# Optimization experiments

Hardware: AMD Instinct MI355X
Metric: run time of the kernel (lower is better)

Reference implementation:

```python
import jax, jax.numpy as jnp
import numpy as np

NUM_HEADS = 16


def setup_inputs() -> dict:
    key = jax.random.key(0)
    ks = jax.random.split(key, 7)
    B, S, H = 4, 2048, 1024
    scale = 1.0 / np.sqrt(H)
    return {
        "hidden_states": jax.random.normal(ks[0], (B, S, H), dtype=jnp.float32),
        "attention_mask": jnp.ones((B, S), dtype=jnp.int32),
        "Wq": jax.random.normal(ks[1], (H, H), dtype=jnp.float32) * scale,
        "bq": jnp.zeros((H,), dtype=jnp.float32),
        "Wk": jax.random.normal(ks[2], (H, H), dtype=jnp.float32) * scale,
        "bk": jnp.zeros((H,), dtype=jnp.float32),
        "Wv": jax.random.normal(ks[3], (H, H), dtype=jnp.float32) * scale,
        "bv": jnp.zeros((H,), dtype=jnp.float32),
    }


def _split_heads(x, n_heads):
    B, S, H = x.shape
    return x.reshape(B, S, n_heads, H // n_heads).transpose(0, 2, 1, 3)  # [B,h,S,d]


def reference(hidden_states, attention_mask, Wq, bq, Wk, bk, Wv, bv):
    B, S, H = hidden_states.shape
    dh = H // NUM_HEADS
    # nn.Linear applies x @ W.T + b
    q = _split_heads(hidden_states @ Wq.T + bq, NUM_HEADS)
    k = _split_heads(hidden_states @ Wk.T + bk, NUM_HEADS)
    v = _split_heads(hidden_states @ Wv.T + bv, NUM_HEADS)
    scores = jnp.einsum("bhqd,bhkd->bhqk", q, k)  # [B,h,S,S]
    # masked_fill with -inf before scaling == masking after scaling
    mask = attention_mask[:, None, None, :] == 0
    scores = jnp.where(mask, -jnp.inf, scores)
    probs = jax.nn.softmax(scores / jnp.sqrt(jnp.float32(dh)), axis=-1)
    out = jnp.einsum("bhqk,bhkd->bhqd", probs, v)  # [B,h,S,d]
    return out.transpose(0, 2, 1, 3).reshape(B, S, H)
```

## Files before the change

### kernel.cpp

```cpp
#include <hip/hip_runtime.h>
#include <hip/hip_bf16.h>
#include <stdint.h>

constexpr int CB  = 4;
constexpr int CS  = 2048;
constexpr int CH  = 1024;
constexpr int CNH = 16;
constexpr int CDH = 64;
constexpr int CM  = CB * CS;

typedef __bf16 bf16x8 __attribute__((ext_vector_type(8)));
typedef float  f32x4  __attribute__((ext_vector_type(4)));

__device__ __forceinline__ unsigned short f2bf(float f) {
    union { float f; unsigned u; } c; c.f = f;
    unsigned u = c.u;
    unsigned r = (u + 0x7fffu + ((u >> 16) & 1u)) >> 16;
    return (unsigned short)r;
}

__device__ __forceinline__ void gl_lds16(const void* g, void* l) {
    __builtin_amdgcn_global_load_lds((const __attribute__((address_space(1))) uint32_t*)g,
                                     (__attribute__((address_space(3))) uint32_t*)l,
                                     16, 0, 0);
}

__device__ __forceinline__ float fexp2(float x) {
#if __has_builtin(__builtin_amdgcn_exp2f)
    return __builtin_amdgcn_exp2f(x);
#else
    return exp2f(x);
#endif
}

__device__ __forceinline__ unsigned cvtpk_bf16(float lo, float hi) {
    unsigned r;
    asm("v_cvt_pk_bf16_f32 %0, %1, %2" : "=v"(r) : "v"(lo), "v"(hi));
    return r;
}

__device__ __forceinline__ void pl32swap(unsigned &a, unsigned &b) {
#if __has_builtin(__builtin_amdgcn_permlane32_swap)
    auto r = __builtin_amdgcn_permlane32_swap(a, b, false, false);
    a = r[0]; b = r[1];
#else
    int lane = threadIdx.x & 63;
    unsigned as = (unsigned)__shfl((int)a, lane ^ 32);
    unsigned bs = (unsigned)__shfl((int)b, lane ^ 32);
    unsigned na = (lane < 32) ? a : bs;
    unsigned nb = (lane < 32) ? as : b;
    a = na; b = nb;
#endif
}

__device__ __forceinline__ void pl16swap(unsigned &a, unsigned &b) {
#if __has_builtin(__builtin_amdgcn_permlane16_swap)
    auto r = __builtin_amdgcn_permlane16_swap(a, b, false, false);
    a = r[0]; b = r[1];
#else
    unsigned as = __builtin_amdgcn_ds_swizzle(a, 0x401F);
    unsigned bs = __builtin_amdgcn_ds_swizzle(b, 0x401F);
    int odd = (threadIdx.x >> 4) & 1;
    unsigned na = odd ? bs : a;
    unsigned nb = odd ? b : as;
    a = na; b = nb;
#endif
}

constexpr float C_SC = 0.125f * 1.44269504f;

__global__ __launch_bounds__(256) void cvt_all(const float* __restrict__ hs,
                                               const float* __restrict__ w0,
                                               const float* __restrict__ w1,
                                               const float* __restrict__ w2,
                                               unsigned short* __restrict__ Xb,
                                               unsigned short* __restrict__ Wb) {
    int z = blockIdx.y;
    const float* src; unsigned short* dst; int n4;
    if (z == 0)      { src = hs; dst = Xb;              n4 = CM * CH / 4; }
    else if (z == 1) { src = w0; dst = Wb;              n4 = CH * CH / 4; }
    else if (z == 2) { src = w1; dst = Wb + CH * CH;    n4 = CH * CH / 4; }
    else             { src = w2; dst = Wb + 2 * CH * CH; n4 = CH * CH / 4; }
    int i = blockIdx.x * blockDim.x + threadIdx.x;
    if (i < n4) {
        float4 v = ((const float4*)src)[i];
        ushort4 o;
        o.x = f2bf(v.x); o.y = f2bf(v.y); o.z = f2bf(v.z); o.w = f2bf(v.w);
        ((ushort4*)dst)[i] = o;
    }
}

__global__ __launch_bounds__(256) void qkv_gemm(
    const unsigned short* __restrict__ Xb,
    const unsigned short* __restrict__ Wb,
    const float* __restrict__ bq, const float* __restrict__ bk, const float* __restrict__ bv,
    unsigned short* __restrict__ Qo,
    unsigned short* __restrict__ Ko,
    unsigned short* __restrict__ Vt)
{
    __shared__ alignas(16) unsigned char smem[34816];
    typedef unsigned short (*tile_t)[128][32];
    tile_t As = (tile_t)smem;
    tile_t Bs = (tile_t)(smem + 16384);
    typedef unsigned short (*ep_t)[136];
    ep_t Ep = (ep_t)smem;

    const int tid  = threadIdx.x;
    const int wave = tid >> 6, lane = tid & 63;
    const int wm = wave >> 1, wn = wave & 1;
    const int col = lane & 15, quad = lane >> 4;
    const int gm = blockIdx.x * 128, gn = blockIdx.y * 128;
    const int z  = blockIdx.z;
    const unsigned short* W = Wb + (size_t)z * CH * CH;

    f32x4 zero = {0.f, 0.f, 0.f, 0.f};
    f32x4 acc[4][4];
    for (int i = 0; i < 4; i++) for (int j = 0; j < 4; j++) acc[i][j] = zero;

    const int arow = lane >> 2;
    const int acol = (lane & 3) * 8;

    auto stage = [&](int buf, int k0) {
        for (int c = 0; c < 2; ++c) {
            int r0 = wave * 32 + c * 16;
            gl_lds16(Xb + (size_t)(gm + r0 + arow) * CH + k0 + acol, &As[buf][r0][0]);
            gl_lds16(W  + (size_t)(gn + r0 + arow) * CH + k0 + acol, &Bs[buf][r0][0]);
        }
    };

    stage(0, 0);
    for (int kk = 0; kk < 32; ++kk) {
        int cur = kk & 1;
        __syncthreads();
        if (kk < 31) stage(cur ^ 1, (kk + 1) * 32);
        bf16x8 af[4], bfm[4];
        for (int i = 0; i < 4; i++)
            af[i] = *(const bf16x8*)&As[cur][wm * 64 + i * 16 + col][quad * 8];
        for (int j = 0; j < 4; j++)
            bfm[j] = *(const bf16x8*)&Bs[cur][wn * 64 + j * 16 + col][quad * 8];
        for (int i = 0; i < 4; i++)
            for (int j = 0; j < 4; j++)
                acc[i][j] = __builtin_amdgcn_mfma_f32_16x16x32_bf16(af[i], bfm[j], acc[i][j], 0, 0, 0);
    }

    __syncthreads();

    const float* bias = (z == 0) ? bq : (z == 1) ? bk : bv;
    const int bb = gm >> 11, ss0 = gm & 2047;
    const int h0 = gn >> 6;

    if (z == 2) {
        for (int j = 0; j < 4; j++) {
            int nl = wn * 64 + j * 16 + col;
            float bias_v = bias[gn + nl];
            for (int i = 0; i < 4; i++) {
                int ml = wm * 64 + i * 16 + quad * 4;
                unsigned d0 = (unsigned)f2bf(acc[i][j][0] + bias_v) |
                              ((unsigned)f2bf(acc[i][j][1] + bias_v) << 16);
                unsigned d1 = (unsigned)f2bf(acc[i][j][2] + bias_v) |
                              ((unsigned)f2bf(acc[i][j][3] + bias_v) << 16);
                *(unsigned*)&Ep[nl][ml]     = d0;
                *(unsigned*)&Ep[nl][ml + 2] = d1;
            }
        }
        __syncthreads();
        for (int p = 0; p < 8; p++) {
            int nl = p * 16 + (tid >> 4);
            int seg = tid & 15;
            uint4 v = *(const uint4*)&Ep[nl][seg * 8];
            int h = h0 + (nl >> 6), d = nl & 63;
            *(uint4*)(Vt + ((size_t)(bb * CNH + h) * CDH + d) * CS + ss0 + seg * 8) = v;
        }
    } else {
        const float mulf = (z == 0) ? C_SC : 1.0f;
        for (int j = 0; j < 4; j++) {
            int nl = wn * 64 + j * 16 + col;
            float bias_v = bias[gn + nl];
            for (int i = 0; i < 4; i++)
                for (int r = 0; r < 4; r++) {
                    int ml = wm * 64 + i * 16 + quad * 4 + r;
                    Ep[ml][nl] = f2bf((acc[i][j][r] + bias_v) * mulf);
                }
        }
        __syncthreads();
        unsigned short* dst01 = (z == 0) ? Qo : Ko;
        for (int p = 0; p < 8; p++) {
            int ml = p * 16 + (tid >> 4);
            int half2 = (tid >> 3) & 1, seg = tid & 7;
            uint4 v = *(const uint4*)&Ep[ml][half2 * 64 + seg * 8];
            int h = h0 + half2;
            *(uint4*)(dst01 + ((size_t)(bb * CNH + h) * CS + ss0 + ml) * CDH + seg * 8) = v;
        }
    }
}

__global__ __launch_bounds__(256, 2) void flash_attn(
    const unsigned short* __restrict__ Q,
    const unsigned short* __restrict__ K,
    const unsigned short* __restrict__ Vt,
    const int* __restrict__ mask,
    float* __restrict__ out)
{
    __shared__ alignas(16) unsigned short Ks[3][64][64];
    __shared__ alignas(16) unsigned short Vs[3][64][64];
    __shared__ unsigned int Mbits[64];

    const int tid  = threadIdx.x;
    const int wave = tid >> 6, lane = tid & 63;
    const int col = lane & 15, quad = lane >> 4;

    const int wg   = blockIdx.y * gridDim.x + blockIdx.x;
    const int nid  = (wg & 7) * 64 + (wg >> 3);
    const int bh   = nid >> 3;
    const int qblk = nid & 7;
    const int bI = bh >> 4, hI = bh & 15;
    const int q0 = qblk * 256 + wave * 64;

    const unsigned short* Qp = Q  + (size_t)bh * CS * CDH;
    const unsigned short* Kp = K  + (size_t)bh * CS * CDH;
    const unsigned short* Vp = Vt + (size_t)bh * CDH * CS;

    {
        const int* mg = mask + bI * CS;
        for (int j = 0; j < 8; j++) {
            int idx = wave * 512 + j * 64 + lane;
            unsigned long long bal = __ballot(mg[idx] != 0);
            if (lane == 0) {
                Mbits[wave * 16 + j * 2]     = (unsigned int)bal;
                Mbits[wave * 16 + j * 2 + 1] = (unsigned int)(bal >> 32);
            }
        }
    }

    bf16x8 aq[4][2];
    for (int i = 0; i < 4; i++)
        for (int ks = 0; ks < 2; ks++)
            aq[i][ks] = *(const bf16x8*)(Qp + (size_t)(q0 + i * 16 + col) * CDH + ks * 32 + quad * 8);

    bf16x8 onesb;
    {
        union { unsigned short u; __bf16 b; } ob; ob.u = 0x3F80;
        for (int j = 0; j < 8; j++) onesb[j] = ob.b;
    }

    f32x4 zero = {0.f, 0.f, 0.f, 0.f};
    f32x4 o[4][4], lfr[4];
    for (int i = 0; i < 4; i++) {
        lfr[i] = zero;
        for (int id = 0; id < 4; id++) o[i][id] = zero;
    }

    const int srow = lane >> 3;
    const int schk = (lane & 7) ^ srow;

    auto stageKV = [&](int buf, int t) {
        const unsigned short* kg = Kp + (size_t)t * 64 * CDH;
        for (int c = 0; c < 2; c++) {
            int r0 = wave * 16 + c * 8;
            gl_lds16(kg + (size_t)(r0 + srow) * CDH + schk * 8, &Ks[buf][r0][0]);
            gl_lds16(Vp + (size_t)(r0 + srow) * CS + t * 64 + schk * 8, &Vs[buf][r0][0]);
        }
    };

    stageKV(0, 0);
    stageKV(1, 1);
    asm volatile("s_waitcnt lgkmcnt(0)" ::: "memory");

    int cur = 0, sp = 2;
    for (int kt = 0; kt < 32; ++kt) {
        if (kt < 31) asm volatile("s_waitcnt vmcnt(4)" ::: "memory");
        else         asm volatile("s_waitcnt vmcnt(0)" ::: "memory");
        asm volatile("s_barrier" ::: "memory");
        if (kt < 30) stageKV(sp, kt + 2);

        f32x4 sfr[4][4];
        for (int i = 0; i < 4; i++) for (int ik = 0; ik < 4; ik++) sfr[i][ik] = zero;
        for (int ks = 0; ks < 2; ks++) {
            bf16x8 bkf[4];
            for (int ik = 0; ik < 4; ik++)
                bkf[ik] = *(const bf16x8*)&Ks[cur][ik * 16 + col][((ks * 4 + quad) ^ (col & 7)) * 8];
            __builtin_amdgcn_s_setprio(1);
            for (int i = 0; i < 4; i++)
                for (int ik = 0; ik < 4; ik++)
                    sfr[i][ik] = __builtin_amdgcn_mfma_f32_16x16x32_bf16(bkf[ik], aq[i][ks], sfr[i][ik], 0, 0, 0);
            __builtin_amdgcn_s_setprio(0);
        }

        unsigned int w0 = Mbits[kt * 2], w1 = Mbits[kt * 2 + 1];
        if ((w0 & w1) != 0xFFFFFFFFu) {
            for (int ik = 0; ik < 4; ik++)
                for (int r = 0; r < 4; r++) {
                    int kv = ik * 16 + quad * 4 + r;
                    unsigned bit = (kv < 32) ? (w0 >> kv) : (w1 >> (kv - 32));
                    float madd = (bit & 1u) ? 0.f : -1.0e30f;
                    for (int i = 0; i < 4; i++) sfr[i][ik][r] += madd;
                }
        }

        bf16x8 bvf[2][4];
        for (int ks = 0; ks < 2; ks++)
            for (int id = 0; id < 4; id++)
                bvf[ks][id] = *(const bf16x8*)&Vs[cur][id * 16 + col][((ks * 4 + quad) ^ (col & 7)) * 8];

        for (int i = 0; i < 4; i++) {
            unsigned c[4][2];
            for (int ik = 0; ik < 4; ik++)
                for (int h = 0; h < 2; h++)
                    c[ik][h] = cvtpk_bf16(fexp2(sfr[i][ik][2 * h]), fexp2(sfr[i][ik][2 * h + 1]));

            unsigned a0 = c[0][0], b0 = c[1][0]; pl32swap(a0, b0); pl16swap(a0, b0);
            unsigned a1 = c[0][1], b1 = c[1][1]; pl32swap(a1, b1); pl16swap(a1, b1);
            unsigned a2 = c[2][0], b2 = c[3][0]; pl32swap(a2, b2); pl16swap(a2, b2);
            unsigned a3 = c[2][1], b3 = c[3][1]; pl32swap(a3, b3); pl16swap(a3, b3);

            uint4 lo4; lo4.x = a0; lo4.y = a1; lo4.z = b0; lo4.w = b1;
            uint4 hi4; hi4.x = a2; hi4.y = a3; hi4.z = b2; hi4.w = b3;
            bf16x8 ap0, ap1;
            __builtin_memcpy(&ap0, &lo4, 16);
            __builtin_memcpy(&ap1, &hi4, 16);

            __builtin_amdgcn_s_setprio(1);
            for (int id = 0; id < 4; id++)
                o[i][id] = __builtin_amdgcn_mfma_f32_16x16x32_bf16(ap0, bvf[0][id], o[i][id], 0, 0, 0);
            lfr[i] = __builtin_amdgcn_mfma_f32_16x16x32_bf16(ap0, onesb, lfr[i], 0, 0, 0);
            for (int id = 0; id < 4; id++)
                o[i][id] = __builtin_amdgcn_mfma_f32_16x16x32_bf16(ap1, bvf[1][id], o[i][id], 0, 0, 0);
            lfr[i] = __builtin_amdgcn_mfma_f32_16x16x32_bf16(ap1, onesb, lfr[i], 0, 0, 0);
            __builtin_amdgcn_s_setprio(0);
        }

        cur = (cur + 1 == 3) ? 0 : cur + 1;
        sp  = (sp  + 1 == 3) ? 0 : sp  + 1;
    }

    for (int i = 0; i < 4; i++)
        for (int r = 0; r < 4; r++) {
            int sI = q0 + i * 16 + quad * 4 + r;
            float inv = 1.0f / lfr[i][r];
            for (int id = 0; id < 4; id++)
                out[((size_t)(bI * CS + sI)) * CH + hI * CDH + id * 16 + col] = o[i][id][r] * inv;
        }
}

extern "C" void kernel_launch(void* const* d_in, const int* in_sizes, int n_in,
                              void* d_out, int out_size, void* d_ws, size_t ws_size,
                              hipStream_t stream) {
    const float* hs  = (const float*)d_in[0];
    const int*  mask = (const int*)d_in[1];
    const float* Wq  = (const float*)d_in[2];
    const float* bq  = (const float*)d_in[3];
    const float* Wk  = (const float*)d_in[4];
    const float* bk  = (const float*)d_in[5];
    const float* Wv  = (const float*)d_in[6];
    const float* bv  = (const float*)d_in[7];
    float* out = (float*)d_out;

    char* ws = (char*)d_ws;
    unsigned short* Xb = (unsigned short*)(ws);
    unsigned short* Wb = (unsigned short*)(ws + 16777216);
    unsigned short* Qb = (unsigned short*)(ws + 23068672);
    unsigned short* Kb = (unsigned short*)(ws + 39845888);
    unsigned short* Vt = (unsigned short*)(ws + 56623104);

    cvt_all<<<dim3(8192, 4), 256, 0, stream>>>(hs, Wq, Wk, Wv, Xb, Wb);

    qkv_gemm<<<dim3(CM / 128, CH / 128, 3), 256, 0, stream>>>(Xb, Wb, bq, bk, bv, Qb, Kb, Vt);

    flash_attn<<<dim3(8, 64), 256, 0, stream>>>(Qb, Kb, Vt, mask, out);
}
```

Measured before the change: 250.8 us.

## Load K/V fragments directly from global into registers, dropping LDS staging

The flash-attention kernel no longer stages K and V tiles through a triple-buffered LDS ring with global_load_lds and barriers. Each wave now loads its MFMA K and V fragments straight from global memory (L2) into registers, software-pipelined so that the next tile's QK^T is issued at the end of the current iteration. This removes LDS traffic and per-tile block barriers. In exchange, the four waves in a block each fetch the same K/V data separately, which raises L2/global load traffic and register pressure.

```diff
diff --git a/kernel.cpp b/kernel.cpp
--- a/kernel.cpp
+++ b/kernel.cpp
@@ -201,8 +201,6 @@
     const int* __restrict__ mask,
     float* __restrict__ out)
 {
-    __shared__ alignas(16) unsigned short Ks[3][64][64];
-    __shared__ alignas(16) unsigned short Vs[3][64][64];
     __shared__ unsigned int Mbits[64];
 
     const int tid  = threadIdx.x;
@@ -216,9 +214,9 @@
     const int bI = bh >> 4, hI = bh & 15;
     const int q0 = qblk * 256 + wave * 64;
 
-    const unsigned short* Qp = Q  + (size_t)bh * CS * CDH;
-    const unsigned short* Kp = K  + (size_t)bh * CS * CDH;
-    const unsigned short* Vp = Vt + (size_t)bh * CDH * CS;
+    const unsigned short* Qp = Q + (size_t)bh * CS * CDH;
+    const char* Kp8 = (const char*)(K  + (size_t)bh * CS * CDH);
+    const char* Vp8 = (const char*)(Vt + (size_t)bh * CDH * CS);
 
     {
         const int* mg = mask + bI * CS;
@@ -231,80 +229,104 @@
             }
         }
     }
+    __syncthreads();
 
     bf16x8 aq[4][2];
+    #pragma unroll
     for (int i = 0; i < 4; i++)
+        #pragma unroll
         for (int ks = 0; ks < 2; ks++)
             aq[i][ks] = *(const bf16x8*)(Qp + (size_t)(q0 + i * 16 + col) * CDH + ks * 32 + quad * 8);
 
     bf16x8 onesb;
     {
         union { unsigned short u; __bf16 b; } ob; ob.u = 0x3F80;
+        #pragma unroll
         for (int j = 0; j < 8; j++) onesb[j] = ob.b;
     }
 
     f32x4 zero = {0.f, 0.f, 0.f, 0.f};
     f32x4 o[4][4], lfr[4];
+    #pragma unroll
     for (int i = 0; i < 4; i++) {
         lfr[i] = zero;
+        #pragma unroll
         for (int id = 0; id < 4; id++) o[i][id] = zero;
     }
 
-    const int srow = lane >> 3;
-    const int schk = (lane & 7) ^ srow;
-
-    auto stageKV = [&](int buf, int t) {
-        const unsigned short* kg = Kp + (size_t)t * 64 * CDH;
-        for (int c = 0; c < 2; c++) {
-            int r0 = wave * 16 + c * 8;
-            gl_lds16(kg + (size_t)(r0 + srow) * CDH + schk * 8, &Ks[buf][r0][0]);
-            gl_lds16(Vp + (size_t)(r0 + srow) * CS + t * 64 + schk * 8, &Vs[buf][r0][0]);
-        }
+    unsigned voKa = (unsigned)(col * 128 + quad * 16);
+    unsigned voKb = voKa + 4096u;
+    unsigned voV0 = (unsigned)(col * 4096 + quad * 16);
+    unsigned voV1 = voV0 + 16u * 4096u;
+    unsigned voV2 = voV0 + 32u * 4096u;
+    unsigned voV3 = voV0 + 48u * 4096u;
+
+    bf16x8 kf[4];
+    bf16x8 vf[2][4];
+    f32x4  sfr[4][4];
+
+    auto ldK = [&](unsigned ks) {
+        kf[0] = *(const bf16x8*)(Kp8 + (voKa + ks * 64u));
+        kf[1] = *(const bf16x8*)(Kp8 + (voKa + 2048u + ks * 64u));
+        kf[2] = *(const bf16x8*)(Kp8 + (voKb + ks * 64u));
+        kf[3] = *(const bf16x8*)(Kp8 + (voKb + 2048u + ks * 64u));
     };
-
-    stageKV(0, 0);
-    stageKV(1, 1);
-    asm volatile("s_waitcnt lgkmcnt(0)" ::: "memory");
-
-    int cur = 0, sp = 2;
+    auto ldV = [&]() {
+        #pragma unroll
+        for (int ks = 0; ks < 2; ks++) {
+            vf[ks][0] = *(const bf16x8*)(Vp8 + (voV0 + (unsigned)ks * 64u));
+            vf[ks][1] = *(const bf16x8*)(Vp8 + (voV1 + (unsigned)ks * 64u));
+            vf[ks][2] = *(const bf16x8*)(Vp8 + (voV2 + (unsigned)ks * 64u));
+            vf[ks][3] = *(const bf16x8*)(Vp8 + (voV3 + (unsigned)ks * 64u));
+        }
+    };
+
+    ldV();
+    ldK(0);
+    #pragma unroll
+    for (int i = 0; i < 4; i++)
+        #pragma unroll
+        for (int ik = 0; ik < 4; ik++) sfr[i][ik] = zero;
+    __builtin_amdgcn_s_setprio(1);
+    #pragma unroll
+    for (int i = 0; i < 4; i++)
+        #pragma unroll
+        for (int ik = 0; ik < 4; ik++)
+            sfr[i][ik] = __builtin_amdgcn_mfma_f32_16x16x32_bf16(kf[ik], aq[i][0], sfr[i][ik], 0, 0, 0);
+    __builtin_amdgcn_s_setprio(0);
+    ldK(1);
+    __builtin_amdgcn_s_setprio(1);
+    #pragma unroll
+    for (int i = 0; i < 4; i++)
+        #pragma unroll
+        for (int ik = 0; ik < 4; ik++)
+            sfr[i][ik] = __builtin_amdgcn_mfma_f32_16x16x32_bf16(kf[ik], aq[i][1], sfr[i][ik], 0, 0, 0);
+    __builtin_amdgcn_s_setprio(0);
+    voKa += 8192u; voKb += 8192u;
+
     for (int kt = 0; kt < 32; ++kt) {
-        if (kt < 31) asm volatile("s_waitcnt vmcnt(4)" ::: "memory");
-        else         asm volatile("s_waitcnt vmcnt(0)" ::: "memory");
-        asm volatile("s_barrier" ::: "memory");
-        if (kt < 30) stageKV(sp, kt + 2);
-
-        f32x4 sfr[4][4];
-        for (int i = 0; i < 4; i++) for (int ik = 0; ik < 4; ik++) sfr[i][ik] = zero;
-        for (int ks = 0; ks < 2; ks++) {
-            bf16x8 bkf[4];
-            for (int ik = 0; ik < 4; ik++)
-                bkf[ik] = *(const bf16x8*)&Ks[cur][ik * 16 + col][((ks * 4 + quad) ^ (col & 7)) * 8];
-            __builtin_amdgcn_s_setprio(1);
-            for (int i = 0; i < 4; i++)
-                for (int ik = 0; ik < 4; ik++)
-                    sfr[i][ik] = __builtin_amdgcn_mfma_f32_16x16x32_bf16(bkf[ik], aq[i][ks], sfr[i][ik], 0, 0, 0);
-            __builtin_amdgcn_s_setprio(0);
-        }
+        if (kt < 31) ldK(0);
 
         unsigned int w0 = Mbits[kt * 2], w1 = Mbits[kt * 2 + 1];
         if ((w0 & w1) != 0xFFFFFFFFu) {
+            #pragma unroll
             for (int ik = 0; ik < 4; ik++)
+                #pragma unroll
                 for (int r = 0; r < 4; r++) {
                     int kv = ik * 16 + quad * 4 + r;
                     unsigned bit = (kv < 32) ? (w0 >> kv) : (w1 >> (kv - 32));
                     float madd = (bit & 1u) ? 0.f : -1.0e30f;
+                    #pragma unroll
                     for (int i = 0; i < 4; i++) sfr[i][ik][r] += madd;
                 }
         }
 
-        bf16x8 bvf[2][4];
-        for (int ks = 0; ks < 2; ks++)
-            for (int id = 0; id < 4; id++)
-                bvf[ks][id] = *(const bf16x8*)&Vs[cur][id * 16 + col][((ks * 4 + quad) ^ (col & 7)) * 8];
-
+        #pragma unroll
         for (int i = 0; i < 4; i++) {
             unsigned c[4][2];
+            #pragma unroll
             for (int ik = 0; ik < 4; ik++)
+                #pragma unroll
                 for (int h = 0; h < 2; h++)
                     c[ik][h] = cvtpk_bf16(fexp2(sfr[i][ik][2 * h]), fexp2(sfr[i][ik][2 * h + 1]));
 
@@ -320,23 +342,51 @@
             __builtin_memcpy(&ap1, &hi4, 16);
 
             __builtin_amdgcn_s_setprio(1);
+            #pragma unroll
             for (int id = 0; id < 4; id++)
-                o[i][id] = __builtin_amdgcn_mfma_f32_16x16x32_bf16(ap0, bvf[0][id], o[i][id], 0, 0, 0);
+                o[i][id] = __builtin_amdgcn_mfma_f32_16x16x32_bf16(ap0, vf[0][id], o[i][id], 0, 0, 0);
             lfr[i] = __builtin_amdgcn_mfma_f32_16x16x32_bf16(ap0, onesb, lfr[i], 0, 0, 0);
+            #pragma unroll
             for (int id = 0; id < 4; id++)
-                o[i][id] = __builtin_amdgcn_mfma_f32_16x16x32_bf16(ap1, bvf[1][id], o[i][id], 0, 0, 0);
+                o[i][id] = __builtin_amdgcn_mfma_f32_16x16x32_bf16(ap1, vf[1][id], o[i][id], 0, 0, 0);
             lfr[i] = __builtin_amdgcn_mfma_f32_16x16x32_bf16(ap1, onesb, lfr[i], 0, 0, 0);
             __builtin_amdgcn_s_setprio(0);
         }
 
-        cur = (cur + 1 == 3) ? 0 : cur + 1;
-        sp  = (sp  + 1 == 3) ? 0 : sp  + 1;
-    }
-
+        if (kt < 31) {
+            voV0 += 128u; voV1 += 128u; voV2 += 128u; voV3 += 128u;
+            ldV();
+
+            #pragma unroll
+            for (int i = 0; i < 4; i++)
+                #pragma unroll
+                for (int ik = 0; ik < 4; ik++) sfr[i][ik] = zero;
+            __builtin_amdgcn_s_setprio(1);
+            #pragma unroll
+            for (int i = 0; i < 4; i++)
+                #pragma unroll
+                for (int ik = 0; ik < 4; ik++)
+                    sfr[i][ik] = __builtin_amdgcn_mfma_f32_16x16x32_bf16(kf[ik], aq[i][0], sfr[i][ik], 0, 0, 0);
+            __builtin_amdgcn_s_setprio(0);
+            ldK(1);
+            __builtin_amdgcn_s_setprio(1);
+            #pragma unroll
+            for (int i = 0; i < 4; i++)
+                #pragma unroll
+                for (int ik = 0; ik < 4; ik++)
+                    sfr[i][ik] = __builtin_amdgcn_mfma_f32_16x16x32_bf16(kf[ik], aq[i][1], sfr[i][ik], 0, 0, 0);
+            __builtin_amdgcn_s_setprio(0);
+            voKa += 8192u; voKb += 8192u;
+        }
+    }
+
+    #pragma unroll
     for (int i = 0; i < 4; i++)
+        #pragma unroll
         for (int r = 0; r < 4; r++) {
             int sI = q0 + i * 16 + quad * 4 + r;
             float inv = 1.0f / lfr[i][r];
+            #pragma unroll
             for (int id = 0; id < 4; id++)
                 out[((size_t)(bI * CS + sI)) * CH + hI * CDH + id * 16 + col] = o[i][id][r] * inv;
         }
```

New measurement: 344.2 us. +37.3%, slower.
